# Performance work log

Hardware: AMD Instinct MI355X
Metric: run time of the kernel (lower is better)

## Reference

```python
import jax, jax.numpy as jnp
import numpy as np

DIM = 64
POS_IN = 34  # 17 joints * 2 coords
POS_HID = 64
ATTN_HID = 4 * DIM


def setup_inputs() -> dict:
    key = jax.random.key(0)
    ks = jax.random.split(key, 11)
    B, T, J, C, N = 2, 16, 17, 3, 128
    BT = B * T
    s = lambda *sh: 1.0 / np.sqrt(sh[-1])
    inp = {
        "x": jax.random.normal(ks[0], (BT, N, DIM), dtype=jnp.float32),
        "pos": jax.random.normal(ks[1], (B, T, J, C, N), dtype=jnp.float32),
        # to_qkv: Linear(dim, 3*dim, bias=False) -> weight [3*dim, dim]
        "w_qkv": jax.random.normal(ks[2], (3 * DIM, DIM), dtype=jnp.float32) * s(DIM, DIM),
        # pos_mlp: Linear(34, 64) -> ReLU -> Linear(64, dim)
        "pm_w1": jax.random.normal(ks[3], (POS_HID, POS_IN), dtype=jnp.float32) * s(1, POS_IN),
        "pm_b1": jnp.zeros((POS_HID,), dtype=jnp.float32),
        "pm_w2": jax.random.normal(ks[4], (DIM, POS_HID), dtype=jnp.float32) * s(1, POS_HID),
        "pm_b2": jnp.zeros((DIM,), dtype=jnp.float32),
        # attn_mlp: Linear(dim, 4*dim) -> ReLU -> Linear(4*dim, dim)
        "am_w1": jax.random.normal(ks[5], (ATTN_HID, DIM), dtype=jnp.float32) * s(1, DIM),
        "am_b1": jnp.zeros((ATTN_HID,), dtype=jnp.float32),
        "am_w2": jax.random.normal(ks[6], (DIM, ATTN_HID), dtype=jnp.float32) * s(1, ATTN_HID),
        "am_b2": jnp.zeros((DIM,), dtype=jnp.float32),
    }
    return inp


def reference(x, pos, w_qkv, pm_w1, pm_b1, pm_w2, pm_b2, am_w1, am_b1, am_w2, am_b2):
    B, T, J, C, N = pos.shape
    # keep first 2 coords, permute (B,T,J,2,N) -> (B,T,N,2,J), flatten to (B*T, N, 2*J)
    p = jnp.transpose(pos[:, :, :, :2, :], (0, 1, 4, 3, 2)).reshape(B * T, N, 2 * J)
    n = x.shape[1]
    qkv = x @ w_qkv.T  # [BT, N, 3*dim]
    q, k, v = jnp.split(qkv, 3, axis=-1)
    # pairwise relative positions [BT, N, N, 2*J]
    rel_pos = p[:, :, None, :] - p[:, None, :, :]
    rel_pos_emb = jax.nn.relu(rel_pos @ pm_w1.T + pm_b1) @ pm_w2.T + pm_b2  # [BT,N,N,dim]
    qk_rel = q[:, :, None, :] - k[:, None, :, :]  # [BT,N,N,dim]
    v_pair = v[:, None, :, :] + rel_pos_emb  # broadcast v over i -> [BT,N,N,dim]
    sim = jax.nn.relu((qk_rel + rel_pos_emb) @ am_w1.T + am_b1) @ am_w2.T + am_b2
    attn = jax.nn.softmax(sim, axis=-2)  # softmax over j
    agg = jnp.einsum("bijd,bijd->bid", attn, v_pair)
    return agg
```

## Files before the change

### kernel.cpp

```cpp
#include <hip/hip_runtime.h>


typedef short short8 __attribute__((ext_vector_type(8)));
typedef float f32x4 __attribute__((ext_vector_type(4)));
typedef float f32x16 __attribute__((ext_vector_type(16)));
typedef unsigned int u32x2 __attribute__((ext_vector_type(2)));

__device__ __forceinline__ unsigned short f2bf(float x) {
  union { float f; unsigned int u; } a; a.f = x;
  unsigned int r = a.u + 0x7fffu + ((a.u >> 16) & 1u);
  return (unsigned short)(r >> 16);
}
__device__ __forceinline__ unsigned int pk2(float a, float b) {
  unsigned int r;
  asm("v_cvt_pk_bf16_f32 %0, %1, %2" : "=v"(r) : "v"(a), "v"(b));
  return r;
}

__device__ __forceinline__ void fill_frag(unsigned short* dst,
    const float* src, int Ksrc, int KC, int idx) {
  int e = idx & 7;
  int lane = (idx >> 3) & 63;
  int kc = (idx >> 9) % KC;
  int mt = idx / (512 * KC);
  int row = mt * 32 + (lane & 31);
  int k = kc * 16 + ((lane >> 5) << 3) + e;
  float v = (k < Ksrc) ? src[row * Ksrc + k] : 0.0f;
  dst[idx] = f2bf(v);
}

#define QKV_BLOCKS 512

__global__ void aux_kernel(const float* __restrict__ wqkv,
    const float* __restrict__ pw1, const float* __restrict__ pw2,
    const float* __restrict__ aw1, const float* __restrict__ aw2,
    const float* __restrict__ x,
    unsigned short* __restrict__ fW1, unsigned short* __restrict__ fW2,
    unsigned short* __restrict__ fA1, unsigned short* __restrict__ fA2,
    float* __restrict__ qkv) {
  int tid = threadIdx.x;
  if (blockIdx.x < QKV_BLOCKS) {
    __shared__ float xs[512];
    int bt = blockIdx.x >> 4, ng = blockIdx.x & 15;
    const float* xb = x + (bt * 128 + ng * 8) * 64;
    xs[tid] = xb[tid];
    xs[tid + 256] = xb[tid + 256];
    __syncthreads();
    if (tid < 192) {
      const float* wr_g = wqkv + tid * 64;
      float wr[64];
#pragma unroll
      for (int k = 0; k < 64; ++k) wr[k] = wr_g[k];
      float* qb = qkv + (size_t)(bt * 128 + ng * 8) * 192 + tid;
#pragma unroll
      for (int n = 0; n < 8; ++n) {
        float acc = 0.f;
#pragma unroll
        for (int k = 0; k < 64; ++k) acc += xs[n * 64 + k] * wr[k];
        qb[n * 192] = acc;
      }
    }
    return;
  }
  int gid = (blockIdx.x - QKV_BLOCKS) * 256 + tid;
  if (gid < 3072) { fill_frag(fW1, pw1, 34, 3, gid); return; }
  gid -= 3072;
  if (gid < 4096) { fill_frag(fW2, pw2, 64, 4, gid); return; }
  gid -= 4096;
  if (gid < 16384) { fill_frag(fA1, aw1, 64, 4, gid); return; }
  gid -= 16384;
  fill_frag(fA2, aw2, 256, 16, gid);
}

__device__ __forceinline__ f32x16 ld16(const float* p, int l) {
  f32x16 r;
#pragma unroll
  for (int q = 0; q < 4; ++q) {
    f32x4 v = *(const f32x4*)(p + 8 * q + ((l >> 5) << 2));
#pragma unroll
    for (int s = 0; s < 4; ++s) r[4 * q + s] = v[s];
  }
  return r;
}

__device__ __forceinline__ void scat(char* buf, int jt, int lc, int lh, int kcb,
                                     f32x16 a, bool relu) {
#pragma unroll
  for (int q = 0; q < 4; ++q) {
    float v0 = a[4*q], v1 = a[4*q+1], v2 = a[4*q+2], v3 = a[4*q+3];
    if (relu) {
      v0 = fmaxf(v0, 0.f); v1 = fmaxf(v1, 0.f);
      v2 = fmaxf(v2, 0.f); v3 = fmaxf(v3, 0.f);
    }
    u32x2 wv; wv[0] = pk2(v0, v1); wv[1] = pk2(v2, v3);
    int kc = kcb + (q >> 1);
    *(u32x2*)(buf + ((kc * 4 + jt) << 10) + (((q & 1) << 5) + lc) * 16 + lh * 8) = wv;
  }
}

#define MFMA32(acc, av, bv) \
  acc = __builtin_amdgcn_mfma_f32_32x32x16_bf16(av, bv, acc, 0, 0, 0)

__global__ __launch_bounds__(256, 4) void main_kernel(
    const float* __restrict__ pos, const float* __restrict__ qkv,
    const unsigned short* __restrict__ fW1, const unsigned short* __restrict__ fW2,
    const unsigned short* __restrict__ fA1, const unsigned short* __restrict__ fA2,
    const float* __restrict__ pb1, const float* __restrict__ pb2,
    const float* __restrict__ ab1, const float* __restrict__ ab2,
    float* __restrict__ out) {
  __shared__ char bufA[16384];
  __shared__ char bufB[16384];
  const int i = blockIdx.x, bt = blockIdx.y;
  const int tid = threadIdx.x;
  const int w = tid >> 6, l = tid & 63;
  const int wm = w >> 1, wn = w & 1;
  const int lc = l & 31, lh = l >> 5;

  short8 w1f[3], w2f[4];
#pragma unroll
  for (int kc = 0; kc < 3; ++kc)
    w1f[kc] = *(const short8*)(fW1 + ((wm * 3 + kc) * 64 + l) * 8);
#pragma unroll
  for (int kc = 0; kc < 4; ++kc)
    w2f[kc] = *(const short8*)(fW2 + ((wm * 4 + kc) * 64 + l) * 8);

#pragma unroll
  for (int it = 0; it < 24; ++it) {
    int idx = tid + (it << 8);
    int f = idx >> 7, j = idx & 127;
    float val = 0.f;
    if (f < 34) {
      int c = (f >= 17) ? 1 : 0;
      int jj = f - 17 * c;
      const float* ps = pos + (((bt * 17 + jj) * 3 + c) << 7);
      val = ps[i] - ps[j];
    }
    int kc = f >> 4, lane = ((f >> 3) & 1) * 32 + (j & 31), jt = j >> 5, e = f & 7;
    *(unsigned short*)(bufA + ((kc * 4 + jt) << 10) + lane * 16 + e * 2) = f2bf(val);
  }
  __syncthreads();

#pragma unroll
  for (int jr = 0; jr < 2; ++jr) {
    int jt = 2 * wn + jr;
    f32x16 acc = ld16(pb1 + wm * 32, l);
#pragma unroll
    for (int kc = 0; kc < 3; ++kc) {
      short8 b = *(const short8*)(bufA + ((kc * 4 + jt) << 10) + l * 16);
      MFMA32(acc, w1f[kc], b);
    }
    scat(bufB, jt, lc, lh, 2 * wm, acc, true);
  }
  __syncthreads();

  unsigned int vpk0[8], vpk1[8];
  const float* qkv_bt = qkv + (size_t)(bt * 128) * 192;
  const float* qp = qkv_bt + i * 192 + wm * 32;
#pragma unroll
  for (int jr = 0; jr < 2; ++jr) {
    int jt = 2 * wn + jr;
    f32x16 e = ld16(pb2 + wm * 32, l);
#pragma unroll
    for (int kc = 0; kc < 4; ++kc) {
      short8 b = *(const short8*)(bufB + ((kc * 4 + jt) << 10) + l * 16);
      MFMA32(e, w2f[kc], b);
    }
    f32x16 qv = ld16(qp, l);
    const float* rp = qkv_bt + (jt * 32 + lc) * 192 + wm * 32;
    f32x16 kk = ld16(rp + 64, l), vv = ld16(rp + 128, l);
    f32x16 u;
#pragma unroll
    for (int r = 0; r < 16; ++r) u[r] = qv[r] - kk[r] + e[r];
#pragma unroll
    for (int s = 0; s < 8; ++s) {
      unsigned int p = pk2(vv[2*s] + e[2*s], vv[2*s+1] + e[2*s+1]);
      if (jr == 0) vpk0[s] = p; else vpk1[s] = p;
    }
    scat(bufA, jt, lc, lh, 2 * wm, u, false);
  }
  __syncthreads();

  f32x16 s0 = ld16(ab2 + wm * 32, l), s1 = s0;
#pragma unroll 1
  for (int hc = 0; hc < 4; ++hc) {
    short8 a1f[4], a2f[4];
#pragma unroll
    for (int kc = 0; kc < 4; ++kc) {
      a1f[kc] = *(const short8*)(fA1 + (((hc * 2 + wm) * 4 + kc) * 64 + l) * 8);
      a2f[kc] = *(const short8*)(fA2 + ((wm * 16 + hc * 4 + kc) * 64 + l) * 8);
    }
#pragma unroll
    for (int jr = 0; jr < 2; ++jr) {
      int jt = 2 * wn + jr;
      f32x16 h = ld16(ab1 + hc * 64 + wm * 32, l);
#pragma unroll
      for (int kc = 0; kc < 4; ++kc) {
        short8 b = *(const short8*)(bufA + ((kc * 4 + jt) << 10) + l * 16);
        MFMA32(h, a1f[kc], b);
      }
      scat(bufB, jt, lc, lh, 2 * wm, h, true);
    }
    __syncthreads();
    {
#pragma unroll
      for (int kc = 0; kc < 4; ++kc) {
        short8 b = *(const short8*)(bufB + ((kc * 4 + 2 * wn) << 10) + l * 16);
        MFMA32(s0, a2f[kc], b);
      }
#pragma unroll
      for (int kc = 0; kc < 4; ++kc) {
        short8 b = *(const short8*)(bufB + ((kc * 4 + 2 * wn + 1) << 10) + l * 16);
        MFMA32(s1, a2f[kc], b);
      }
    }
    __syncthreads();
  }

  float* red = (float*)bufA;
#pragma unroll
  for (int q = 0; q < 4; ++q) {
#pragma unroll
    for (int sp = 0; sp < 2; ++sp) {
      int r0 = 4 * q + 2 * sp;
      int pi = 2 * q + sp;
      float x00 = __expf(s0[r0]),     x10 = __expf(s1[r0]);
      float x01 = __expf(s0[r0 + 1]), x11 = __expf(s1[r0 + 1]);
      float v00 = __uint_as_float(vpk0[pi] << 16);
      float v01 = __uint_as_float(vpk0[pi] & 0xffff0000u);
      float v10 = __uint_as_float(vpk1[pi] << 16);
      float v11 = __uint_as_float(vpk1[pi] & 0xffff0000u);
      float pdA = x00 + x10, pnA = x00 * v00 + x10 * v10;
      float pdB = x01 + x11, pnB = x01 * v01 + x11 * v11;
#pragma unroll
      for (int m = 1; m <= 16; m <<= 1) {
        pdA += __shfl_xor(pdA, m); pnA += __shfl_xor(pnA, m);
        pdB += __shfl_xor(pdB, m); pnB += __shfl_xor(pnB, m);
      }
      if (lc == 0) {
        int dA = wm * 32 + (r0 & 3) + 8 * (r0 >> 2) + 4 * lh;
        red[wn * 64 + dA] = pdA;       red[128 + wn * 64 + dA] = pnA;
        red[wn * 64 + dA + 1] = pdB;   red[128 + wn * 64 + dA + 1] = pnB;
      }
    }
  }
  __syncthreads();
  if (tid < 64) {
    float den = red[tid] + red[64 + tid];
    float num = red[128 + tid] + red[192 + tid];
    out[(bt * 128 + i) * 64 + tid] = num / den;
  }
}

extern "C" void kernel_launch(void* const* d_in, const int* in_sizes, int n_in,
                              void* d_out, int out_size, void* d_ws, size_t ws_size,
                              hipStream_t stream) {
  const float* x    = (const float*)d_in[0];
  const float* pos  = (const float*)d_in[1];
  const float* wqkv = (const float*)d_in[2];
  const float* pw1  = (const float*)d_in[3];
  const float* pb1  = (const float*)d_in[4];
  const float* pw2  = (const float*)d_in[5];
  const float* pb2  = (const float*)d_in[6];
  const float* aw1  = (const float*)d_in[7];
  const float* ab1  = (const float*)d_in[8];
  const float* aw2  = (const float*)d_in[9];
  const float* ab2  = (const float*)d_in[10];
  float* out = (float*)d_out;
  char* ws = (char*)d_ws;

  float* qkv = (float*)ws;
  unsigned short* fW1 = (unsigned short*)(ws + 3145728);
  unsigned short* fW2 = (unsigned short*)(ws + 3151872);
  unsigned short* fA1 = (unsigned short*)(ws + 3160064);
  unsigned short* fA2 = (unsigned short*)(ws + 3192832);

  hipLaunchKernelGGL(aux_kernel, dim3(QKV_BLOCKS + 156), dim3(256), 0, stream,
                     wqkv, pw1, pw2, aw1, aw2, x, fW1, fW2, fA1, fA2, qkv);
  hipLaunchKernelGGL(main_kernel, dim3(128, 32), dim3(256), 0, stream,
                     pos, qkv, fW1, fW2, fA1, fA2, pb1, pb2, ab1, ab2, out);
}
```

Baseline: 168.5 us.

## Keep MLP intermediates in registers via permlane swap instead of LDS staging

Each wave now owns 32 j-columns for all 64 output rows, so MFMA accumulator outputs are turned directly into bf16 B-operand fragments with v_permlane32_swap. This removes the LDS scatter/gather buffers and the per-stage __syncthreads between the pos-MLP, attn-MLP layers. Weight fragments are read from global memory (cache) inside the loops rather than held per-wave. The QKV projection is also regrouped to 32 rows per block, and launch bounds drop to 3 blocks per CU to allow more registers.

```diff
diff --git a/kernel.cpp b/kernel.cpp
--- a/kernel.cpp
+++ b/kernel.cpp
@@ -4,7 +4,9 @@
 typedef short short8 __attribute__((ext_vector_type(8)));
 typedef float f32x4 __attribute__((ext_vector_type(4)));
 typedef float f32x16 __attribute__((ext_vector_type(16)));
-typedef unsigned int u32x2 __attribute__((ext_vector_type(2)));
+typedef unsigned int u32x4 __attribute__((ext_vector_type(4)));
+
+union frag_u { short8 s; u32x4 u; };
 
 __device__ __forceinline__ unsigned short f2bf(float x) {
   union { float f; unsigned int u; } a; a.f = x;
@@ -29,7 +31,7 @@
   dst[idx] = f2bf(v);
 }
 
-#define QKV_BLOCKS 512
+#define QKV_BLOCKS 128
 
 __global__ void aux_kernel(const float* __restrict__ wqkv,
     const float* __restrict__ pw1, const float* __restrict__ pw2,
@@ -40,24 +42,27 @@
     float* __restrict__ qkv) {
   int tid = threadIdx.x;
   if (blockIdx.x < QKV_BLOCKS) {
-    __shared__ float xs[512];
-    int bt = blockIdx.x >> 4, ng = blockIdx.x & 15;
-    const float* xb = x + (bt * 128 + ng * 8) * 64;
-    xs[tid] = xb[tid];
-    xs[tid + 256] = xb[tid + 256];
+    __shared__ float xs[32 * 64];
+    int bt = blockIdx.x >> 2, nq = blockIdx.x & 3;
+    const float* xb = x + (bt * 128 + nq * 32) * 64;
+#pragma unroll
+    for (int o = 0; o < 8; ++o) xs[tid + o * 256] = xb[tid + o * 256];
     __syncthreads();
     if (tid < 192) {
       const float* wr_g = wqkv + tid * 64;
       float wr[64];
 #pragma unroll
       for (int k = 0; k < 64; ++k) wr[k] = wr_g[k];
-      float* qb = qkv + (size_t)(bt * 128 + ng * 8) * 192 + tid;
-#pragma unroll
-      for (int n = 0; n < 8; ++n) {
-        float acc = 0.f;
-#pragma unroll
-        for (int k = 0; k < 64; ++k) acc += xs[n * 64 + k] * wr[k];
-        qb[n * 192] = acc;
+      float* qb = qkv + (size_t)(bt * 128 + nq * 32) * 192 + tid;
+      for (int n = 0; n < 32; n += 2) {
+        float a0 = 0.f, a1 = 0.f;
+#pragma unroll
+        for (int k = 0; k < 64; ++k) {
+          a0 += xs[n * 64 + k] * wr[k];
+          a1 += xs[n * 64 + 64 + k] * wr[k];
+        }
+        qb[n * 192] = a0;
+        qb[n * 192 + 192] = a1;
       }
     }
     return;
@@ -83,170 +88,141 @@
   return r;
 }
 
-__device__ __forceinline__ void scat(char* buf, int jt, int lc, int lh, int kcb,
-                                     f32x16 a, bool relu) {
-#pragma unroll
-  for (int q = 0; q < 4; ++q) {
-    float v0 = a[4*q], v1 = a[4*q+1], v2 = a[4*q+2], v3 = a[4*q+3];
+__device__ __forceinline__ void c2b(f32x16 c, short8* out, bool relu) {
+#pragma unroll
+  for (int kk = 0; kk < 2; ++kk) {
+    float a0 = c[8*kk+0], a1 = c[8*kk+1], a2 = c[8*kk+2], a3 = c[8*kk+3];
+    float a4 = c[8*kk+4], a5 = c[8*kk+5], a6 = c[8*kk+6], a7 = c[8*kk+7];
     if (relu) {
-      v0 = fmaxf(v0, 0.f); v1 = fmaxf(v1, 0.f);
-      v2 = fmaxf(v2, 0.f); v3 = fmaxf(v3, 0.f);
-    }
-    u32x2 wv; wv[0] = pk2(v0, v1); wv[1] = pk2(v2, v3);
-    int kc = kcb + (q >> 1);
-    *(u32x2*)(buf + ((kc * 4 + jt) << 10) + (((q & 1) << 5) + lc) * 16 + lh * 8) = wv;
+      a0 = fmaxf(a0, 0.f); a1 = fmaxf(a1, 0.f); a2 = fmaxf(a2, 0.f); a3 = fmaxf(a3, 0.f);
+      a4 = fmaxf(a4, 0.f); a5 = fmaxf(a5, 0.f); a6 = fmaxf(a6, 0.f); a7 = fmaxf(a7, 0.f);
+    }
+    unsigned u0 = pk2(a0, a1), u1 = pk2(a2, a3), u2 = pk2(a4, a5), u3 = pk2(a6, a7);
+    asm("v_permlane32_swap_b32 %0, %1" : "+v"(u0), "+v"(u2));
+    asm("v_permlane32_swap_b32 %0, %1" : "+v"(u1), "+v"(u3));
+    frag_u fu; fu.u[0] = u0; fu.u[1] = u1; fu.u[2] = u2; fu.u[3] = u3;
+    out[kk] = fu.s;
   }
 }
 
 #define MFMA32(acc, av, bv) \
   acc = __builtin_amdgcn_mfma_f32_32x32x16_bf16(av, bv, acc, 0, 0, 0)
-
-__global__ __launch_bounds__(256, 4) void main_kernel(
+#define AF(ptr, idx) (*(const short8*)((ptr) + (size_t)(idx) * 512 + (size_t)l * 8))
+
+__global__ __launch_bounds__(256, 3) void main_kernel(
     const float* __restrict__ pos, const float* __restrict__ qkv,
     const unsigned short* __restrict__ fW1, const unsigned short* __restrict__ fW2,
     const unsigned short* __restrict__ fA1, const unsigned short* __restrict__ fA2,
     const float* __restrict__ pb1, const float* __restrict__ pb2,
     const float* __restrict__ ab1, const float* __restrict__ ab2,
     float* __restrict__ out) {
-  __shared__ char bufA[16384];
-  __shared__ char bufB[16384];
+  __shared__ float red[512];
   const int i = blockIdx.x, bt = blockIdx.y;
   const int tid = threadIdx.x;
   const int w = tid >> 6, l = tid & 63;
-  const int wm = w >> 1, wn = w & 1;
-  const int lc = l & 31, lh = l >> 5;
-
-  short8 w1f[3], w2f[4];
-#pragma unroll
-  for (int kc = 0; kc < 3; ++kc)
-    w1f[kc] = *(const short8*)(fW1 + ((wm * 3 + kc) * 64 + l) * 8);
-#pragma unroll
-  for (int kc = 0; kc < 4; ++kc)
-    w2f[kc] = *(const short8*)(fW2 + ((wm * 4 + kc) * 64 + l) * 8);
-
-#pragma unroll
-  for (int it = 0; it < 24; ++it) {
-    int idx = tid + (it << 8);
-    int f = idx >> 7, j = idx & 127;
-    float val = 0.f;
-    if (f < 34) {
-      int c = (f >= 17) ? 1 : 0;
-      int jj = f - 17 * c;
-      const float* ps = pos + (((bt * 17 + jj) * 3 + c) << 7);
-      val = ps[i] - ps[j];
-    }
-    int kc = f >> 4, lane = ((f >> 3) & 1) * 32 + (j & 31), jt = j >> 5, e = f & 7;
-    *(unsigned short*)(bufA + ((kc * 4 + jt) << 10) + lane * 16 + e * 2) = f2bf(val);
-  }
-  __syncthreads();
-
-#pragma unroll
-  for (int jr = 0; jr < 2; ++jr) {
-    int jt = 2 * wn + jr;
-    f32x16 acc = ld16(pb1 + wm * 32, l);
-#pragma unroll
-    for (int kc = 0; kc < 3; ++kc) {
-      short8 b = *(const short8*)(bufA + ((kc * 4 + jt) << 10) + l * 16);
-      MFMA32(acc, w1f[kc], b);
-    }
-    scat(bufB, jt, lc, lh, 2 * wm, acc, true);
-  }
-  __syncthreads();
-
-  unsigned int vpk0[8], vpk1[8];
+  const int lc = l & 31, h5 = l >> 5;
+  const int j = w * 32 + lc;
+
+  short8 x1f[3];
+#pragma unroll
+  for (int kc = 0; kc < 3; ++kc) {
+    frag_u fu;
+#pragma unroll
+    for (int wo = 0; wo < 4; ++wo) {
+      float v0 = 0.f, v1 = 0.f;
+      int f0 = kc * 16 + h5 * 8 + 2 * wo;
+      if (f0 < 34) {
+        int c = (f0 >= 17) ? 1 : 0;
+        const float* ps = pos + (((bt * 17 + (f0 - 17 * c)) * 3 + c) << 7);
+        v0 = ps[i] - ps[j];
+      }
+      int f1 = f0 + 1;
+      if (f1 < 34) {
+        int c = (f1 >= 17) ? 1 : 0;
+        const float* ps = pos + (((bt * 17 + (f1 - 17 * c)) * 3 + c) << 7);
+        v1 = ps[i] - ps[j];
+      }
+      fu.u[wo] = pk2(v0, v1);
+    }
+    x1f[kc] = fu.s;
+  }
+
+  short8 h1b[4];
+#pragma unroll
+  for (int mt = 0; mt < 2; ++mt) {
+    f32x16 acc = ld16(pb1 + mt * 32, l);
+#pragma unroll
+    for (int kc = 0; kc < 3; ++kc) MFMA32(acc, AF(fW1, mt * 3 + kc), x1f[kc]);
+    c2b(acc, &h1b[2 * mt], true);
+  }
+
+  unsigned vpk[16];
+  short8 ub[4];
   const float* qkv_bt = qkv + (size_t)(bt * 128) * 192;
-  const float* qp = qkv_bt + i * 192 + wm * 32;
-#pragma unroll
-  for (int jr = 0; jr < 2; ++jr) {
-    int jt = 2 * wn + jr;
-    f32x16 e = ld16(pb2 + wm * 32, l);
-#pragma unroll
-    for (int kc = 0; kc < 4; ++kc) {
-      short8 b = *(const short8*)(bufB + ((kc * 4 + jt) << 10) + l * 16);
-      MFMA32(e, w2f[kc], b);
-    }
-    f32x16 qv = ld16(qp, l);
-    const float* rp = qkv_bt + (jt * 32 + lc) * 192 + wm * 32;
-    f32x16 kk = ld16(rp + 64, l), vv = ld16(rp + 128, l);
+  const float* rp = qkv_bt + j * 192;
+#pragma unroll
+  for (int mt = 0; mt < 2; ++mt) {
+    f32x16 e = ld16(pb2 + mt * 32, l);
+#pragma unroll
+    for (int kc = 0; kc < 4; ++kc) MFMA32(e, AF(fW2, mt * 4 + kc), h1b[kc]);
+    f32x16 qv = ld16(qkv_bt + i * 192 + mt * 32, l);
+    f32x16 kk = ld16(rp + 64 + mt * 32, l);
+    f32x16 vv = ld16(rp + 128 + mt * 32, l);
     f32x16 u;
 #pragma unroll
     for (int r = 0; r < 16; ++r) u[r] = qv[r] - kk[r] + e[r];
 #pragma unroll
-    for (int s = 0; s < 8; ++s) {
-      unsigned int p = pk2(vv[2*s] + e[2*s], vv[2*s+1] + e[2*s+1]);
-      if (jr == 0) vpk0[s] = p; else vpk1[s] = p;
-    }
-    scat(bufA, jt, lc, lh, 2 * wm, u, false);
-  }
-  __syncthreads();
-
-  f32x16 s0 = ld16(ab2 + wm * 32, l), s1 = s0;
+    for (int s = 0; s < 8; ++s)
+      vpk[mt * 8 + s] = pk2(vv[2 * s] + e[2 * s], vv[2 * s + 1] + e[2 * s + 1]);
+    c2b(u, &ub[2 * mt], false);
+  }
+
+  f32x16 s0 = ld16(ab2, l), s1 = ld16(ab2 + 32, l);
 #pragma unroll 1
   for (int hc = 0; hc < 4; ++hc) {
-    short8 a1f[4], a2f[4];
+    short8 h2b[4];
+#pragma unroll
+    for (int mt = 0; mt < 2; ++mt) {
+      f32x16 h = ld16(ab1 + hc * 64 + mt * 32, l);
+#pragma unroll
+      for (int kc = 0; kc < 4; ++kc) MFMA32(h, AF(fA1, (hc * 2 + mt) * 4 + kc), ub[kc]);
+      c2b(h, &h2b[2 * mt], true);
+    }
 #pragma unroll
     for (int kc = 0; kc < 4; ++kc) {
-      a1f[kc] = *(const short8*)(fA1 + (((hc * 2 + wm) * 4 + kc) * 64 + l) * 8);
-      a2f[kc] = *(const short8*)(fA2 + ((wm * 16 + hc * 4 + kc) * 64 + l) * 8);
-    }
-#pragma unroll
-    for (int jr = 0; jr < 2; ++jr) {
-      int jt = 2 * wn + jr;
-      f32x16 h = ld16(ab1 + hc * 64 + wm * 32, l);
-#pragma unroll
-      for (int kc = 0; kc < 4; ++kc) {
-        short8 b = *(const short8*)(bufA + ((kc * 4 + jt) << 10) + l * 16);
-        MFMA32(h, a1f[kc], b);
-      }
-      scat(bufB, jt, lc, lh, 2 * wm, h, true);
-    }
-    __syncthreads();
-    {
-#pragma unroll
-      for (int kc = 0; kc < 4; ++kc) {
-        short8 b = *(const short8*)(bufB + ((kc * 4 + 2 * wn) << 10) + l * 16);
-        MFMA32(s0, a2f[kc], b);
-      }
-#pragma unroll
-      for (int kc = 0; kc < 4; ++kc) {
-        short8 b = *(const short8*)(bufB + ((kc * 4 + 2 * wn + 1) << 10) + l * 16);
-        MFMA32(s1, a2f[kc], b);
-      }
-    }
-    __syncthreads();
-  }
-
-  float* red = (float*)bufA;
-#pragma unroll
-  for (int q = 0; q < 4; ++q) {
-#pragma unroll
-    for (int sp = 0; sp < 2; ++sp) {
-      int r0 = 4 * q + 2 * sp;
-      int pi = 2 * q + sp;
-      float x00 = __expf(s0[r0]),     x10 = __expf(s1[r0]);
-      float x01 = __expf(s0[r0 + 1]), x11 = __expf(s1[r0 + 1]);
-      float v00 = __uint_as_float(vpk0[pi] << 16);
-      float v01 = __uint_as_float(vpk0[pi] & 0xffff0000u);
-      float v10 = __uint_as_float(vpk1[pi] << 16);
-      float v11 = __uint_as_float(vpk1[pi] & 0xffff0000u);
-      float pdA = x00 + x10, pnA = x00 * v00 + x10 * v10;
-      float pdB = x01 + x11, pnB = x01 * v01 + x11 * v11;
+      MFMA32(s0, AF(fA2, hc * 4 + kc), h2b[kc]);
+      MFMA32(s1, AF(fA2, 16 + hc * 4 + kc), h2b[kc]);
+    }
+  }
+
+#pragma unroll
+  for (int mt = 0; mt < 2; ++mt) {
+    f32x16 sc = mt ? s1 : s0;
+#pragma unroll
+    for (int pi = 0; pi < 8; ++pi) {
+      int r0 = 2 * pi;
+      float x0 = __expf(sc[r0]), x1 = __expf(sc[r0 + 1]);
+      unsigned pv = vpk[mt * 8 + pi];
+      float v0 = __uint_as_float(pv << 16);
+      float v1 = __uint_as_float(pv & 0xffff0000u);
+      float pd0 = x0, pn0 = x0 * v0;
+      float pd1 = x1, pn1 = x1 * v1;
 #pragma unroll
       for (int m = 1; m <= 16; m <<= 1) {
-        pdA += __shfl_xor(pdA, m); pnA += __shfl_xor(pnA, m);
-        pdB += __shfl_xor(pdB, m); pnB += __shfl_xor(pnB, m);
+        pd0 += __shfl_xor(pd0, m); pn0 += __shfl_xor(pn0, m);
+        pd1 += __shfl_xor(pd1, m); pn1 += __shfl_xor(pn1, m);
       }
       if (lc == 0) {
-        int dA = wm * 32 + (r0 & 3) + 8 * (r0 >> 2) + 4 * lh;
-        red[wn * 64 + dA] = pdA;       red[128 + wn * 64 + dA] = pnA;
-        red[wn * 64 + dA + 1] = pdB;   red[128 + wn * 64 + dA + 1] = pnB;
+        int d0 = mt * 32 + (r0 & 3) + 8 * (r0 >> 2) + 4 * h5;
+        red[w * 128 + d0] = pd0;          red[w * 128 + 64 + d0] = pn0;
+        red[w * 128 + d0 + 1] = pd1;      red[w * 128 + 64 + d0 + 1] = pn1;
       }
     }
   }
   __syncthreads();
   if (tid < 64) {
-    float den = red[tid] + red[64 + tid];
-    float num = red[128 + tid] + red[192 + tid];
+    float den = red[tid] + red[128 + tid] + red[256 + tid] + red[384 + tid];
+    float num = red[64 + tid] + red[192 + tid] + red[320 + tid] + red[448 + tid];
     out[(bt * 128 + i) * 64 + tid] = num / den;
   }
 }
```

Result: slower. 258.1 us (+53.2%).
